# Optimization experiments

Hardware: AMD Instinct MI355X
Metric: run time of the kernel (lower is better)

The kernel has to match this reference:

```python
import jax, jax.numpy as jnp
import numpy as np

N_NODES = 100000
N_EDGES = 1600000
D = 128
N_REL = 237  # embedding table has N_REL+1 rows, row 0 = padding (zero)


def setup_inputs() -> dict:
    key = jax.random.key(0)
    k1, k2, k3, k4, k5, k6 = jax.random.split(key, 6)
    stdv = 1.0 / np.sqrt(D)
    inputs = {
        "input": jax.random.normal(k1, (N_NODES, D), dtype=jnp.float32),
        "edge_index": jax.random.randint(k2, (2, N_EDGES), 0, N_NODES, dtype=jnp.int64),
        "rel": jax.random.randint(k3, (N_EDGES,), 0, N_REL + 1, dtype=jnp.int64),
        "n": N_NODES,
        "weight": jax.random.uniform(k4, (D, D), dtype=jnp.float32, minval=-stdv, maxval=stdv),
        "alpha_emb": jax.random.normal(k5, (N_REL + 1, 1), dtype=jnp.float32),
        "bias": jax.random.uniform(k6, (D,), dtype=jnp.float32, minval=-stdv, maxval=stdv),
    }
    return inputs


def reference(input, edge_index, rel, n, weight, alpha_emb, bias):
    # padding_idx=0: row 0 of the relation-weight table is zero
    alpha_tab = alpha_emb.at[0].set(0.0)
    alp = alpha_tab[rel, 0]                       # [E] per-edge scalar weight
    support = input @ weight                      # [N, D]
    row, col = edge_index[0], edge_index[1]
    # output = (A + A^T) @ support without materializing a sparse matrix:
    # A contributes alp * support[col] into rows `row`; A^T the reverse.
    msg_fwd = alp[:, None] * support[col]         # [E, D]
    msg_bwd = alp[:, None] * support[row]         # [E, D]
    out = jax.ops.segment_sum(msg_fwd, row, num_segments=n)
    out = out + jax.ops.segment_sum(msg_bwd, col, num_segments=n)
    return out + bias
```

## Files before the change

### kernel.cpp

```cpp
#include <hip/hip_runtime.h>
#include <hip/hip_bf16.h>

typedef __attribute__((ext_vector_type(8))) short bf16x8;
typedef __attribute__((ext_vector_type(4))) float f32x4;

static __device__ __forceinline__ unsigned short f2bf(float f) {
    unsigned u = __float_as_uint(f);
    unsigned r = (u + 0x7FFFu + ((u >> 16) & 1u)) >> 16;
    return (unsigned short)r;
}
static __device__ __forceinline__ float bfLo(unsigned d) { return __uint_as_float(d << 16); }
static __device__ __forceinline__ float bfHi(unsigned d) { return __uint_as_float(d & 0xFFFF0000u); }

#define PART_BLOCKS 128
#define PART_TPB 1024
#define BUCKET 32
#define CAP_SHIFT 11
#define CAP (1u << CAP_SHIFT)
#define CHUNK 2048

__global__ __launch_bounds__(256, 2) void mfma_gemm_kernel(const float* __restrict__ A,
                                                           const float* __restrict__ W,
                                                           unsigned short* __restrict__ S,
                                                           int N) {
    __shared__ float sW[128 * 128];
    const int t = threadIdx.x;
    const int w = t >> 6;
    const int l = t & 63;
    const int l15 = l & 15;
    const int lq = l >> 4;
    const int row0 = blockIdx.x * 128;

    for (int i = t * 4; i < 128 * 128; i += 256 * 4)
        *(float4*)&sW[i] = *(const float4*)&W[i];
    __syncthreads();

    bf16x8 bfrag[8][4];
#pragma unroll
    for (int tc = 0; tc < 8; ++tc) {
#pragma unroll
        for (int ks = 0; ks < 4; ++ks) {
            const int c = tc * 16 + l15;
            const int k0 = ks * 32 + lq * 8;
            bf16x8 f;
#pragma unroll
            for (int i = 0; i < 8; ++i)
                f[i] = (short)f2bf(sW[(k0 + i) * 128 + c]);
            bfrag[tc][ks] = f;
        }
    }

    f32x4 acc[2][8];
#pragma unroll
    for (int rt = 0; rt < 2; ++rt)
#pragma unroll
        for (int tc = 0; tc < 8; ++tc)
            acc[rt][tc] = (f32x4){0.f, 0.f, 0.f, 0.f};

    const int wrow = row0 + w * 32;
#pragma unroll
    for (int ks = 0; ks < 4; ++ks) {
        bf16x8 afrag[2];
#pragma unroll
        for (int rt = 0; rt < 2; ++rt) {
            const int r = wrow + rt * 16 + l15;
            bf16x8 f = (bf16x8){0, 0, 0, 0, 0, 0, 0, 0};
            if (r < N) {
                const float* p = &A[(size_t)r * 128 + ks * 32 + lq * 8];
                float4 v0 = *(const float4*)p;
                float4 v1 = *(const float4*)(p + 4);
                f[0] = (short)f2bf(v0.x); f[1] = (short)f2bf(v0.y);
                f[2] = (short)f2bf(v0.z); f[3] = (short)f2bf(v0.w);
                f[4] = (short)f2bf(v1.x); f[5] = (short)f2bf(v1.y);
                f[6] = (short)f2bf(v1.z); f[7] = (short)f2bf(v1.w);
            }
            afrag[rt] = f;
        }
#pragma unroll
        for (int rt = 0; rt < 2; ++rt)
#pragma unroll
            for (int tc = 0; tc < 8; ++tc)
                acc[rt][tc] = __builtin_amdgcn_mfma_f32_16x16x32_bf16(
                    afrag[rt], bfrag[tc][ks], acc[rt][tc], 0, 0, 0);
    }

#pragma unroll
    for (int rt = 0; rt < 2; ++rt) {
#pragma unroll
        for (int j = 0; j < 4; ++j) {
            const int r = wrow + rt * 16 + lq * 4 + j;
            if (r < N) {
                unsigned short* Sp = S + (size_t)r * 128;
#pragma unroll
                for (int tc = 0; tc < 8; ++tc)
                    Sp[tc * 16 + l15] = f2bf(acc[rt][tc][j]);
            }
        }
    }
}

__global__ __launch_bounds__(PART_TPB) void partition_kernel(
        const int* __restrict__ ei, const int* __restrict__ rel,
        unsigned* __restrict__ cursor, unsigned* __restrict__ rec,
        int E, int nbuck, long long chunk) {
    extern __shared__ unsigned sh[];
    unsigned* hist = sh;
    unsigned* base = sh + nbuck;
    const long long start = (long long)blockIdx.x * chunk;
    long long end = start + chunk; if (end > E) end = E;
    const int t = threadIdx.x;

    for (int i = t; i < nbuck; i += PART_TPB) hist[i] = 0u;
    __syncthreads();
    for (long long e = start + t; e < end; e += PART_TPB) {
        unsigned r = (unsigned)ei[e];
        unsigned c = (unsigned)ei[e + E];
        atomicAdd(&hist[r >> 5], 1u);
        atomicAdd(&hist[c >> 5], 1u);
    }
    __syncthreads();
    for (int i = t; i < nbuck; i += PART_TPB) {
        unsigned cn = hist[i];
        base[i] = cn ? atomicAdd(&cursor[i], cn) : 0u;
        hist[i] = 0u;
    }
    __syncthreads();
    for (long long e = start + t; e < end; e += PART_TPB) {
        unsigned r = (unsigned)ei[e];
        unsigned c = (unsigned)ei[e + E];
        unsigned rr = (unsigned)rel[e];
        unsigned b1 = r >> 5;
        unsigned l1 = atomicAdd(&hist[b1], 1u);
        unsigned p1 = base[b1] + l1;
        if (p1 < CAP)
            rec[((size_t)b1 << CAP_SHIFT) + p1] = c | (rr << 17) | ((r & 31u) << 25);
        unsigned b2 = c >> 5;
        unsigned l2 = atomicAdd(&hist[b2], 1u);
        unsigned p2 = base[b2] + l2;
        if (p2 < CAP)
            rec[((size_t)b2 << CAP_SHIFT) + p2] = r | (rr << 17) | ((c & 31u) << 25);
    }
}

static __device__ __forceinline__ void accum_run(const unsigned short* __restrict__ support,
                                                 const unsigned* sorted,
                                                 const float* aLds,
                                                 unsigned s0, unsigned cq, int lane,
                                                 float4& acc) {
    unsigned j = 0;
    for (; j + 8 <= cq; j += 8) {
        unsigned rr[8]; uint2 qq[8]; float aa[8];
#pragma unroll
        for (int u = 0; u < 8; ++u) rr[u] = sorted[s0 + j + u];
#pragma unroll
        for (int u = 0; u < 8; ++u)
            qq[u] = ((const uint2*)(support + (size_t)(rr[u] & 0x1FFFFu) * 128))[lane];
#pragma unroll
        for (int u = 0; u < 8; ++u) aa[u] = aLds[(rr[u] >> 17) & 0xFFu];
#pragma unroll
        for (int u = 0; u < 8; ++u) {
            acc.x += aa[u] * bfLo(qq[u].x);
            acc.y += aa[u] * bfHi(qq[u].x);
            acc.z += aa[u] * bfLo(qq[u].y);
            acc.w += aa[u] * bfHi(qq[u].y);
        }
    }
    for (; j < cq; ++j) {
        unsigned r0 = sorted[s0 + j];
        uint2 q0 = ((const uint2*)(support + (size_t)(r0 & 0x1FFFFu) * 128))[lane];
        float a0 = aLds[(r0 >> 17) & 0xFFu];
        acc.x += a0 * bfLo(q0.x); acc.y += a0 * bfHi(q0.x);
        acc.z += a0 * bfLo(q0.y); acc.w += a0 * bfHi(q0.y);
    }
}

__global__ __launch_bounds__(256) void gather_bucket_kernel(const unsigned short* __restrict__ support,
                                                            const unsigned* __restrict__ rec,
                                                            const unsigned* __restrict__ cnt,
                                                            const float* __restrict__ alpha,
                                                            const float* __restrict__ bias,
                                                            float* __restrict__ out,
                                                            int N, int nAlpha) {
    __shared__ float aLds[256];
    __shared__ unsigned sorted[CHUNK];
    __shared__ unsigned scnt[BUCKET], sstart[BUCKET], scur[BUCKET];

    const int t = threadIdx.x;
    const int b = blockIdx.x;
    const int lane = t & 31;
    const int hw = t >> 5;

    {
        float a = 0.f;
        if (t > 0 && t < nAlpha) a = alpha[t];
        aLds[t] = a;
    }
    const float4 b4 = *(const float4*)&bias[lane * 4];

    float4 acc0 = make_float4(0.f, 0.f, 0.f, 0.f);
    float4 acc1 = make_float4(0.f, 0.f, 0.f, 0.f);
    float4 acc2 = make_float4(0.f, 0.f, 0.f, 0.f);
    float4 acc3 = make_float4(0.f, 0.f, 0.f, 0.f);

    const unsigned start = (unsigned)b << CAP_SHIFT;
    unsigned total = cnt[b];
    if (total > CAP) total = CAP;

    for (unsigned cb = 0; cb < total; cb += CHUNK) {
        const unsigned cc = min((unsigned)CHUNK, total - cb);
        __syncthreads();
        if (t < BUCKET) scnt[t] = 0u;
        __syncthreads();

        unsigned r[8];
#pragma unroll
        for (int k = 0; k < 8; ++k) {
            unsigned i = (unsigned)(k * 256 + t);
            r[k] = 0xFFFFFFFFu;
            if (i < cc) {
                r[k] = rec[start + cb + i];
                atomicAdd(&scnt[r[k] >> 25], 1u);
            }
        }
        __syncthreads();

        if (t < BUCKET) {
            unsigned c = scnt[t];
            unsigned x = c;
#pragma unroll
            for (int d = 1; d < BUCKET; d <<= 1) {
                unsigned y = __shfl_up(x, d, BUCKET);
                if (t >= d) x += y;
            }
            sstart[t] = x - c;
            scur[t] = x - c;
        }
        __syncthreads();

#pragma unroll
        for (int k = 0; k < 8; ++k) {
            if (r[k] != 0xFFFFFFFFu) {
                unsigned dl = r[k] >> 25;
                unsigned pos = atomicAdd(&scur[dl], 1u);
                sorted[pos] = r[k];
            }
        }
        __syncthreads();

        accum_run(support, sorted, aLds, sstart[hw * 4 + 0], scnt[hw * 4 + 0], lane, acc0);
        accum_run(support, sorted, aLds, sstart[hw * 4 + 1], scnt[hw * 4 + 1], lane, acc1);
        accum_run(support, sorted, aLds, sstart[hw * 4 + 2], scnt[hw * 4 + 2], lane, acc2);
        accum_run(support, sorted, aLds, sstart[hw * 4 + 3], scnt[hw * 4 + 3], lane, acc3);
    }

    const int node0 = b * BUCKET + hw * 4;
#define WRITE_NODE(Q, ACC)                                                          \
    {                                                                               \
        int node = node0 + (Q);                                                     \
        if (node < N) {                                                             \
            float4 o = make_float4(ACC.x + b4.x, ACC.y + b4.y,                      \
                                   ACC.z + b4.z, ACC.w + b4.w);                     \
            *(float4*)&out[(size_t)node * 128 + lane * 4] = o;                      \
        }                                                                           \
    }
    WRITE_NODE(0, acc0)
    WRITE_NODE(1, acc1)
    WRITE_NODE(2, acc2)
    WRITE_NODE(3, acc3)
#undef WRITE_NODE
}

__global__ __launch_bounds__(256) void gemm_kernel(const float* __restrict__ A,
                                                   const float* __restrict__ W,
                                                   unsigned short* __restrict__ S,
                                                   int N) {
    __shared__ float sIn[128][33];
    __shared__ float sW[32][128];
    const int tid = threadIdx.x;
    const int tx = tid & 15;
    const int ty = tid >> 4;
    const int row0 = blockIdx.x * 128;
    float acc[8][8];
#pragma unroll
    for (int i = 0; i < 8; ++i)
#pragma unroll
        for (int j = 0; j < 8; ++j) acc[i][j] = 0.f;
    for (int kc = 0; kc < 128; kc += 32) {
#pragma unroll
        for (int p = 0; p < 4; ++p) {
            int r = p * 32 + (tid >> 3);
            int q = tid & 7;
            int grow = row0 + r;
            float4 v = make_float4(0.f, 0.f, 0.f, 0.f);
            if (grow < N) v = *(const float4*)&A[(size_t)grow * 128 + kc + q * 4];
            sIn[r][q * 4 + 0] = v.x; sIn[r][q * 4 + 1] = v.y;
            sIn[r][q * 4 + 2] = v.z; sIn[r][q * 4 + 3] = v.w;
        }
#pragma unroll
        for (int p = 0; p < 4; ++p) {
            int kr = p * 8 + (tid >> 5);
            int c4 = tid & 31;
            *(float4*)&sW[kr][c4 * 4] = *(const float4*)&W[(size_t)(kc + kr) * 128 + c4 * 4];
        }
        __syncthreads();
#pragma unroll
        for (int k = 0; k < 32; ++k) {
            float a[8];
#pragma unroll
            for (int i = 0; i < 8; ++i) a[i] = sIn[ty * 8 + i][k];
            float4 w0 = *(float4*)&sW[k][tx * 4];
            float4 w1 = *(float4*)&sW[k][64 + tx * 4];
#pragma unroll
            for (int i = 0; i < 8; ++i) {
                acc[i][0] += a[i] * w0.x; acc[i][1] += a[i] * w0.y;
                acc[i][2] += a[i] * w0.z; acc[i][3] += a[i] * w0.w;
                acc[i][4] += a[i] * w1.x; acc[i][5] += a[i] * w1.y;
                acc[i][6] += a[i] * w1.z; acc[i][7] += a[i] * w1.w;
            }
        }
        __syncthreads();
    }
#pragma unroll
    for (int i = 0; i < 8; ++i) {
        int grow = row0 + ty * 8 + i;
        if (grow < N) {
            unsigned short* Sp = S + (size_t)grow * 128;
            unsigned a0 = (unsigned)f2bf(acc[i][0]) | ((unsigned)f2bf(acc[i][1]) << 16);
            unsigned a1 = (unsigned)f2bf(acc[i][2]) | ((unsigned)f2bf(acc[i][3]) << 16);
            unsigned a2 = (unsigned)f2bf(acc[i][4]) | ((unsigned)f2bf(acc[i][5]) << 16);
            unsigned a3 = (unsigned)f2bf(acc[i][6]) | ((unsigned)f2bf(acc[i][7]) << 16);
            *(uint2*)&Sp[tx * 4] = make_uint2(a0, a1);
            *(uint2*)&Sp[64 + tx * 4] = make_uint2(a2, a3);
        }
    }
}

__global__ __launch_bounds__(256) void init_out_kernel(float* __restrict__ out,
                                                       const float* __restrict__ bias,
                                                       long long total4) {
    long long i = (long long)blockIdx.x * blockDim.x + threadIdx.x;
    if (i >= total4) return;
    float4 b = ((const float4*)bias)[(int)(i & 31)];
    ((float4*)out)[i] = b;
}

__global__ __launch_bounds__(256) void scatter_kernel(const unsigned short* __restrict__ support,
                                                      const int* __restrict__ ei,
                                                      const int* __restrict__ rel,
                                                      const float* __restrict__ alpha,
                                                      float* __restrict__ out,
                                                      int E) {
    long long tid = (long long)blockIdx.x * blockDim.x + threadIdx.x;
    long long mid = tid >> 5;
    if (mid >= 2LL * E) return;
    int lane4 = (int)(tid & 31);
    int dst = ei[mid];
    long long ms = (mid < E) ? mid + E : mid - E;
    int src = ei[ms];
    int e = (int)((mid < E) ? mid : mid - E);
    int rr = rel[e];
    float alp = (rr == 0) ? 0.f : alpha[rr];
    if (alp == 0.f) return;
    uint2 q = ((const uint2*)(support + (size_t)src * 128))[lane4];
    float* o = &out[(size_t)dst * 128 + lane4 * 4];
    atomicAdd(o + 0, alp * bfLo(q.x));
    atomicAdd(o + 1, alp * bfHi(q.x));
    atomicAdd(o + 2, alp * bfLo(q.y));
    atomicAdd(o + 3, alp * bfHi(q.y));
}

extern "C" void kernel_launch(void* const* d_in, const int* in_sizes, int n_in,
                              void* d_out, int out_size, void* d_ws, size_t ws_size,
                              hipStream_t stream) {
    const float* input  = (const float*)d_in[0];
    const int*   ei     = (const int*)d_in[1];
    const int*   rel    = (const int*)d_in[2];
    const float* weight = (const float*)d_in[4];
    const float* alpha  = (const float*)d_in[5];
    const float* bias   = (const float*)d_in[6];
    float*       out    = (float*)d_out;

    const int N = in_sizes[0] / 128;
    const int E = in_sizes[2];
    const int nAlpha = in_sizes[5];
    const long long M = 2LL * E;
    const int nbuck = (N + BUCKET - 1) / BUCKET;

    char* ws = (char*)d_ws;
    size_t supB = ((size_t)N * 128 * 2 + 255) & ~(size_t)255;
    const size_t curB = ((size_t)nbuck * 4 + 255) & ~(size_t)255;
    unsigned short* support = (unsigned short*)ws;
    unsigned* cursor = (unsigned*)(ws + supB);
    unsigned* rec    = (unsigned*)(ws + supB + curB);
    const size_t need = supB + curB + ((size_t)nbuck << CAP_SHIFT) * 4;

    const int gemmBlocks = (N + 127) / 128;
    const bool okMain = (ws_size >= need) && (N <= (1 << 17)) && (nAlpha <= 256) &&
                        (nbuck <= 4096) && ((long long)(M / (nbuck ? nbuck : 1)) * 2 <= (long long)CAP);

    if (okMain) {
        const long long chunk = ((long long)E + PART_BLOCKS - 1) / PART_BLOCKS;
        hipMemsetAsync(cursor, 0, (size_t)nbuck * 4, stream);
        partition_kernel<<<PART_BLOCKS, PART_TPB, 2 * nbuck * 4, stream>>>(
            ei, rel, cursor, rec, E, nbuck, chunk);
        mfma_gemm_kernel<<<gemmBlocks, 256, 0, stream>>>(input, weight, support, N);
        gather_bucket_kernel<<<nbuck, 256, 0, stream>>>(
            support, rec, cursor, alpha, bias, out, N, nAlpha);
    } else {
        gemm_kernel<<<gemmBlocks, 256, 0, stream>>>(input, weight, support, N);
        long long total4 = (long long)N * 32;
        init_out_kernel<<<(int)((total4 + 255) / 256), 256, 0, stream>>>(out, bias, total4);
        long long tthreads = M * 32;
        scatter_kernel<<<(int)((tthreads + 255) / 256), 256, 0, stream>>>(
            support, ei, rel, alpha, out, E);
    }
}
```

Before: 201.0 us.

## Replace global atomic bucket cursors with per-block partitioned segments and offset table

The partition kernel now does a local prefix scan and writes each block's records into its own contiguous region, recording per-bucket offsets, instead of claiming slots in a fixed-capacity global bucket array through global atomics. The gather kernel reads the 128 per-block segments for its bucket, scans their lengths, and stages the records in shared memory before the local sort. This drops the memset, the global atomic contention and the capacity limit on bucket size. In exchange the gather does scattered reads of many small segments, makes more block-wide syncs for the scans, and uses more LDS per block.

```diff
diff --git a/kernel.cpp b/kernel.cpp
--- a/kernel.cpp
+++ b/kernel.cpp
@@ -12,11 +12,9 @@
 static __device__ __forceinline__ float bfLo(unsigned d) { return __uint_as_float(d << 16); }
 static __device__ __forceinline__ float bfHi(unsigned d) { return __uint_as_float(d & 0xFFFF0000u); }
 
-#define PART_BLOCKS 128
+#define PB 128
 #define PART_TPB 1024
 #define BUCKET 32
-#define CAP_SHIFT 11
-#define CAP (1u << CAP_SHIFT)
 #define CHUNK 2048
 
 __global__ __launch_bounds__(256, 2) void mfma_gemm_kernel(const float* __restrict__ A,
@@ -101,14 +99,16 @@
 
 __global__ __launch_bounds__(PART_TPB) void partition_kernel(
         const int* __restrict__ ei, const int* __restrict__ rel,
-        unsigned* __restrict__ cursor, unsigned* __restrict__ rec,
-        int E, int nbuck, long long chunk) {
+        unsigned* __restrict__ offs, unsigned* __restrict__ rec,
+        int E, int nbuck, int chunkE, int chunkRecs) {
     extern __shared__ unsigned sh[];
     unsigned* hist = sh;
-    unsigned* base = sh + nbuck;
-    const long long start = (long long)blockIdx.x * chunk;
-    long long end = start + chunk; if (end > E) end = E;
+    unsigned* cur  = sh + nbuck;
+    unsigned* tmp  = cur + nbuck;
     const int t = threadIdx.x;
+    const int p = blockIdx.x;
+    const long long start = (long long)p * chunkE;
+    long long end = start + chunkE; if (end > E) end = E;
 
     for (int i = t; i < nbuck; i += PART_TPB) hist[i] = 0u;
     __syncthreads();
@@ -119,26 +119,47 @@
         atomicAdd(&hist[c >> 5], 1u);
     }
     __syncthreads();
-    for (int i = t; i < nbuck; i += PART_TPB) {
-        unsigned cn = hist[i];
-        base[i] = cn ? atomicAdd(&cursor[i], cn) : 0u;
-        hist[i] = 0u;
-    }
-    __syncthreads();
+
+    const int per = (nbuck + PART_TPB - 1) / PART_TPB;
+    const int base0 = t * per;
+    unsigned lsum = 0;
+    for (int i = 0; i < per; ++i) {
+        int idx = base0 + i;
+        if (idx < nbuck) lsum += hist[idx];
+    }
+    tmp[t] = lsum;
+    __syncthreads();
+    for (int d = 1; d < PART_TPB; d <<= 1) {
+        unsigned x = (t >= d) ? tmp[t - d] : 0u;
+        __syncthreads();
+        tmp[t] += x;
+        __syncthreads();
+    }
+    unsigned run = (t == 0) ? 0u : tmp[t - 1];
+    for (int i = 0; i < per; ++i) {
+        int idx = base0 + i;
+        if (idx < nbuck) {
+            unsigned c0 = hist[idx];
+            hist[idx] = run;
+            cur[idx] = run;
+            run += c0;
+        }
+    }
+    __syncthreads();
+
+    unsigned* orow = offs + (size_t)p * (nbuck + 1);
+    for (int i = t; i < nbuck; i += PART_TPB) orow[i] = hist[i];
+    if (t == 0) orow[nbuck] = tmp[PART_TPB - 1];
+
+    unsigned* rbase = rec + (size_t)p * chunkRecs;
     for (long long e = start + t; e < end; e += PART_TPB) {
         unsigned r = (unsigned)ei[e];
         unsigned c = (unsigned)ei[e + E];
         unsigned rr = (unsigned)rel[e];
-        unsigned b1 = r >> 5;
-        unsigned l1 = atomicAdd(&hist[b1], 1u);
-        unsigned p1 = base[b1] + l1;
-        if (p1 < CAP)
-            rec[((size_t)b1 << CAP_SHIFT) + p1] = c | (rr << 17) | ((r & 31u) << 25);
-        unsigned b2 = c >> 5;
-        unsigned l2 = atomicAdd(&hist[b2], 1u);
-        unsigned p2 = base[b2] + l2;
-        if (p2 < CAP)
-            rec[((size_t)b2 << CAP_SHIFT) + p2] = r | (rr << 17) | ((c & 31u) << 25);
+        unsigned p1 = atomicAdd(&cur[r >> 5], 1u);
+        rbase[p1] = c | (rr << 17) | ((r & 31u) << 25);
+        unsigned p2 = atomicAdd(&cur[c >> 5], 1u);
+        rbase[p2] = r | (rr << 17) | ((c & 31u) << 25);
     }
 }
 
@@ -176,13 +197,18 @@
 
 __global__ __launch_bounds__(256) void gather_bucket_kernel(const unsigned short* __restrict__ support,
                                                             const unsigned* __restrict__ rec,
-                                                            const unsigned* __restrict__ cnt,
+                                                            const unsigned* __restrict__ offs,
                                                             const float* __restrict__ alpha,
                                                             const float* __restrict__ bias,
                                                             float* __restrict__ out,
-                                                            int N, int nAlpha) {
+                                                            int N, int nAlpha, int nbuck,
+                                                            int chunkRecs) {
     __shared__ float aLds[256];
+    __shared__ unsigned raw[CHUNK];
     __shared__ unsigned sorted[CHUNK];
+    __shared__ unsigned segS[PB];
+    __shared__ unsigned segL[PB];
+    __shared__ unsigned segD[PB];
     __shared__ unsigned scnt[BUCKET], sstart[BUCKET], scur[BUCKET];
 
     const int t = threadIdx.x;
@@ -197,29 +223,48 @@
     }
     const float4 b4 = *(const float4*)&bias[lane * 4];
 
+    if (t < PB) {
+        const unsigned* orow = offs + (size_t)t * (nbuck + 1);
+        unsigned s = orow[b];
+        unsigned e2 = orow[b + 1];
+        segS[t] = (unsigned)t * (unsigned)chunkRecs + s;
+        segL[t] = e2 - s;
+    }
+    __syncthreads();
+    if (t < PB) segD[t] = segL[t];
+    __syncthreads();
+    for (int d = 1; d < PB; d <<= 1) {
+        unsigned x = (t < PB && t >= d) ? segD[t - d] : 0u;
+        __syncthreads();
+        if (t < PB) segD[t] += x;
+        __syncthreads();
+    }
+    const unsigned T = segD[PB - 1];
+
     float4 acc0 = make_float4(0.f, 0.f, 0.f, 0.f);
     float4 acc1 = make_float4(0.f, 0.f, 0.f, 0.f);
     float4 acc2 = make_float4(0.f, 0.f, 0.f, 0.f);
     float4 acc3 = make_float4(0.f, 0.f, 0.f, 0.f);
 
-    const unsigned start = (unsigned)b << CAP_SHIFT;
-    unsigned total = cnt[b];
-    if (total > CAP) total = CAP;
-
-    for (unsigned cb = 0; cb < total; cb += CHUNK) {
-        const unsigned cc = min((unsigned)CHUNK, total - cb);
+    const int seg = t & (PB - 1);
+    const int half = t >> 7;
+
+    for (unsigned w0 = 0; w0 < T; w0 += CHUNK) {
+        const unsigned w1 = min(w0 + (unsigned)CHUNK, T);
+        const unsigned cc = w1 - w0;
         __syncthreads();
         if (t < BUCKET) scnt[t] = 0u;
         __syncthreads();
 
-        unsigned r[8];
-#pragma unroll
-        for (int k = 0; k < 8; ++k) {
-            unsigned i = (unsigned)(k * 256 + t);
-            r[k] = 0xFFFFFFFFu;
-            if (i < cc) {
-                r[k] = rec[start + cb + i];
-                atomicAdd(&scnt[r[k] >> 25], 1u);
+        {
+            unsigned incl = segD[seg], len = segL[seg];
+            unsigned gs = incl - len;
+            unsigned lo = gs > w0 ? gs : w0;
+            unsigned hi = incl < w1 ? incl : w1;
+            for (unsigned g = lo + half; g < hi; g += 2) {
+                unsigned v = rec[segS[seg] + (g - gs)];
+                raw[g - w0] = v;
+                atomicAdd(&scnt[v >> 25], 1u);
             }
         }
         __syncthreads();
@@ -237,12 +282,12 @@
         }
         __syncthreads();
 
-#pragma unroll
         for (int k = 0; k < 8; ++k) {
-            if (r[k] != 0xFFFFFFFFu) {
-                unsigned dl = r[k] >> 25;
-                unsigned pos = atomicAdd(&scur[dl], 1u);
-                sorted[pos] = r[k];
+            unsigned i = (unsigned)(k * 256 + t);
+            if (i < cc) {
+                unsigned v = raw[i];
+                unsigned pos = atomicAdd(&scur[v >> 25], 1u);
+                sorted[pos] = v;
             }
         }
         __syncthreads();
@@ -386,26 +431,28 @@
     const long long M = 2LL * E;
     const int nbuck = (N + BUCKET - 1) / BUCKET;
 
+    const int chunkE = (E + PB - 1) / PB;
+    const int chunkRecs = 2 * chunkE;
+
     char* ws = (char*)d_ws;
-    size_t supB = ((size_t)N * 128 * 2 + 255) & ~(size_t)255;
-    const size_t curB = ((size_t)nbuck * 4 + 255) & ~(size_t)255;
+    const size_t supB  = ((size_t)N * 128 * 2 + 255) & ~(size_t)255;
+    const size_t offsB = ((size_t)PB * (nbuck + 1) * 4 + 255) & ~(size_t)255;
     unsigned short* support = (unsigned short*)ws;
-    unsigned* cursor = (unsigned*)(ws + supB);
-    unsigned* rec    = (unsigned*)(ws + supB + curB);
-    const size_t need = supB + curB + ((size_t)nbuck << CAP_SHIFT) * 4;
+    unsigned* offs = (unsigned*)(ws + supB);
+    unsigned* rec  = (unsigned*)(ws + supB + offsB);
+    const size_t need = supB + offsB + (size_t)PB * chunkRecs * 4;
 
     const int gemmBlocks = (N + 127) / 128;
+    const size_t partShmem = (size_t)(2 * nbuck + PART_TPB) * 4;
     const bool okMain = (ws_size >= need) && (N <= (1 << 17)) && (nAlpha <= 256) &&
-                        (nbuck <= 4096) && ((long long)(M / (nbuck ? nbuck : 1)) * 2 <= (long long)CAP);
+                        (nbuck <= 4096);
 
     if (okMain) {
-        const long long chunk = ((long long)E + PART_BLOCKS - 1) / PART_BLOCKS;
-        hipMemsetAsync(cursor, 0, (size_t)nbuck * 4, stream);
-        partition_kernel<<<PART_BLOCKS, PART_TPB, 2 * nbuck * 4, stream>>>(
-            ei, rel, cursor, rec, E, nbuck, chunk);
+        partition_kernel<<<PB, PART_TPB, partShmem, stream>>>(
+            ei, rel, offs, rec, E, nbuck, chunkE, chunkRecs);
         mfma_gemm_kernel<<<gemmBlocks, 256, 0, stream>>>(input, weight, support, N);
         gather_bucket_kernel<<<nbuck, 256, 0, stream>>>(
-            support, rec, cursor, alpha, bias, out, N, nAlpha);
+            support, rec, offs, alpha, bias, out, N, nAlpha, nbuck, chunkRecs);
     } else {
         gemm_kernel<<<gemmBlocks, 256, 0, stream>>>(input, weight, support, N);
         long long total4 = (long long)N * 32;
```

Measured after the change: 202.9 us. Within noise of the previous version (+1.0%).

## Replace two-pass LDS histogram partition with sub-bucketed global atomic cursors

Applied to the files above, without the earlier changes.

The partition kernel drops its shared-memory histogram, per-block reservation and second pass. Each edge endpoint now takes a slot with a global atomicAdd on one of 8 sub-cursors per bucket, chosen by block index, and writes into a fixed 256-entry sub-segment. The gather kernel builds a prefix over the sub-segment counts and maps each linear index to its sub-segment before loading. This removes one pass over the edges and the LDS reservation step, at the cost of many contended global atomics and a tighter per-sub-segment capacity that could drop records if a sub-bucket overflows.

```diff
diff --git a/kernel.cpp b/kernel.cpp
--- a/kernel.cpp
+++ b/kernel.cpp
@@ -12,11 +12,12 @@
 static __device__ __forceinline__ float bfLo(unsigned d) { return __uint_as_float(d << 16); }
 static __device__ __forceinline__ float bfHi(unsigned d) { return __uint_as_float(d & 0xFFFF0000u); }
 
-#define PART_BLOCKS 128
+#define PART_BLOCKS 256
 #define PART_TPB 1024
 #define BUCKET 32
+#define NSUB 8
+#define SUBCAP 256
 #define CAP_SHIFT 11
-#define CAP (1u << CAP_SHIFT)
 #define CHUNK 2048
 
 __global__ __launch_bounds__(256, 2) void mfma_gemm_kernel(const float* __restrict__ A,
@@ -101,44 +102,26 @@
 
 __global__ __launch_bounds__(PART_TPB) void partition_kernel(
         const int* __restrict__ ei, const int* __restrict__ rel,
-        unsigned* __restrict__ cursor, unsigned* __restrict__ rec,
-        int E, int nbuck, long long chunk) {
-    extern __shared__ unsigned sh[];
-    unsigned* hist = sh;
-    unsigned* base = sh + nbuck;
+        unsigned* __restrict__ cur, unsigned* __restrict__ rec,
+        int E, long long chunk) {
+    const int sub = blockIdx.x & (NSUB - 1);
     const long long start = (long long)blockIdx.x * chunk;
     long long end = start + chunk; if (end > E) end = E;
-    const int t = threadIdx.x;
-
-    for (int i = t; i < nbuck; i += PART_TPB) hist[i] = 0u;
-    __syncthreads();
-    for (long long e = start + t; e < end; e += PART_TPB) {
-        unsigned r = (unsigned)ei[e];
-        unsigned c = (unsigned)ei[e + E];
-        atomicAdd(&hist[r >> 5], 1u);
-        atomicAdd(&hist[c >> 5], 1u);
-    }
-    __syncthreads();
-    for (int i = t; i < nbuck; i += PART_TPB) {
-        unsigned cn = hist[i];
-        base[i] = cn ? atomicAdd(&cursor[i], cn) : 0u;
-        hist[i] = 0u;
-    }
-    __syncthreads();
-    for (long long e = start + t; e < end; e += PART_TPB) {
+
+    for (long long e = start + threadIdx.x; e < end; e += PART_TPB) {
         unsigned r = (unsigned)ei[e];
         unsigned c = (unsigned)ei[e + E];
         unsigned rr = (unsigned)rel[e];
         unsigned b1 = r >> 5;
-        unsigned l1 = atomicAdd(&hist[b1], 1u);
-        unsigned p1 = base[b1] + l1;
-        if (p1 < CAP)
-            rec[((size_t)b1 << CAP_SHIFT) + p1] = c | (rr << 17) | ((r & 31u) << 25);
+        unsigned p1 = atomicAdd(&cur[b1 * NSUB + sub], 1u);
+        if (p1 < SUBCAP)
+            rec[((size_t)b1 << CAP_SHIFT) + (sub << 8) + p1] =
+                c | (rr << 17) | ((r & 31u) << 25);
         unsigned b2 = c >> 5;
-        unsigned l2 = atomicAdd(&hist[b2], 1u);
-        unsigned p2 = base[b2] + l2;
-        if (p2 < CAP)
-            rec[((size_t)b2 << CAP_SHIFT) + p2] = r | (rr << 17) | ((c & 31u) << 25);
+        unsigned p2 = atomicAdd(&cur[b2 * NSUB + sub], 1u);
+        if (p2 < SUBCAP)
+            rec[((size_t)b2 << CAP_SHIFT) + (sub << 8) + p2] =
+                r | (rr << 17) | ((c & 31u) << 25);
     }
 }
 
@@ -184,6 +167,7 @@
     __shared__ float aLds[256];
     __shared__ unsigned sorted[CHUNK];
     __shared__ unsigned scnt[BUCKET], sstart[BUCKET], scur[BUCKET];
+    __shared__ unsigned segD[NSUB + 1];
 
     const int t = threadIdx.x;
     const int b = blockIdx.x;
@@ -195,19 +179,30 @@
         if (t > 0 && t < nAlpha) a = alpha[t];
         aLds[t] = a;
     }
+    if (t == 0) {
+        unsigned run = 0;
+        segD[0] = 0;
+#pragma unroll
+        for (int s = 0; s < NSUB; ++s) {
+            unsigned c = cnt[b * NSUB + s];
+            if (c > SUBCAP) c = SUBCAP;
+            run += c;
+            segD[s + 1] = run;
+        }
+    }
     const float4 b4 = *(const float4*)&bias[lane * 4];
+    __syncthreads();
+    const unsigned T = segD[NSUB];
 
     float4 acc0 = make_float4(0.f, 0.f, 0.f, 0.f);
     float4 acc1 = make_float4(0.f, 0.f, 0.f, 0.f);
     float4 acc2 = make_float4(0.f, 0.f, 0.f, 0.f);
     float4 acc3 = make_float4(0.f, 0.f, 0.f, 0.f);
 
-    const unsigned start = (unsigned)b << CAP_SHIFT;
-    unsigned total = cnt[b];
-    if (total > CAP) total = CAP;
-
-    for (unsigned cb = 0; cb < total; cb += CHUNK) {
-        const unsigned cc = min((unsigned)CHUNK, total - cb);
+    const unsigned base = (unsigned)b << CAP_SHIFT;
+
+    for (unsigned w0 = 0; w0 < T; w0 += CHUNK) {
+        const unsigned cc = min((unsigned)CHUNK, T - w0);
         __syncthreads();
         if (t < BUCKET) scnt[t] = 0u;
         __syncthreads();
@@ -218,7 +213,11 @@
             unsigned i = (unsigned)(k * 256 + t);
             r[k] = 0xFFFFFFFFu;
             if (i < cc) {
-                r[k] = rec[start + cb + i];
+                unsigned g = w0 + i;
+                unsigned s = 0;
+#pragma unroll
+                for (int j = 1; j < NSUB; ++j) s += (g >= segD[j]) ? 1u : 0u;
+                r[k] = rec[base + (s << 8) + (g - segD[s])];
                 atomicAdd(&scnt[r[k] >> 25], 1u);
             }
         }
@@ -387,25 +386,26 @@
     const int nbuck = (N + BUCKET - 1) / BUCKET;
 
     char* ws = (char*)d_ws;
-    size_t supB = ((size_t)N * 128 * 2 + 255) & ~(size_t)255;
-    const size_t curB = ((size_t)nbuck * 4 + 255) & ~(size_t)255;
+    const size_t supB = ((size_t)N * 128 * 2 + 255) & ~(size_t)255;
+    const size_t curB = ((size_t)nbuck * NSUB * 4 + 255) & ~(size_t)255;
     unsigned short* support = (unsigned short*)ws;
-    unsigned* cursor = (unsigned*)(ws + supB);
-    unsigned* rec    = (unsigned*)(ws + supB + curB);
+    unsigned* cur = (unsigned*)(ws + supB);
+    unsigned* rec = (unsigned*)(ws + supB + curB);
     const size_t need = supB + curB + ((size_t)nbuck << CAP_SHIFT) * 4;
 
     const int gemmBlocks = (N + 127) / 128;
+    const long long meanSub = M / ((long long)(nbuck ? nbuck : 1) * NSUB);
     const bool okMain = (ws_size >= need) && (N <= (1 << 17)) && (nAlpha <= 256) &&
-                        (nbuck <= 4096) && ((long long)(M / (nbuck ? nbuck : 1)) * 2 <= (long long)CAP);
+                        (nbuck <= 4096) && (meanSub * 3 <= 2 * SUBCAP);
 
     if (okMain) {
         const long long chunk = ((long long)E + PART_BLOCKS - 1) / PART_BLOCKS;
-        hipMemsetAsync(cursor, 0, (size_t)nbuck * 4, stream);
-        partition_kernel<<<PART_BLOCKS, PART_TPB, 2 * nbuck * 4, stream>>>(
-            ei, rel, cursor, rec, E, nbuck, chunk);
+        hipMemsetAsync(cur, 0, (size_t)nbuck * NSUB * 4, stream);
+        partition_kernel<<<PART_BLOCKS, PART_TPB, 0, stream>>>(
+            ei, rel, cur, rec, E, chunk);
         mfma_gemm_kernel<<<gemmBlocks, 256, 0, stream>>>(input, weight, support, N);
         gather_bucket_kernel<<<nbuck, 256, 0, stream>>>(
-            support, rec, cursor, alpha, bias, out, N, nAlpha);
+            support, rec, cur, alpha, bias, out, N, nAlpha);
     } else {
         gemm_kernel<<<gemmBlocks, 256, 0, stream>>>(input, weight, support, N);
         long long total4 = (long long)N * 32;
```

Result: slower. 322.1 us (+60.3%).
